# Optimization experiments

Measured on AMD Instinct MI355X. Metric: run time of the kernel, lower is better.

The kernel has to match this reference:

```python
import jax, jax.numpy as jnp
import numpy as np

N_NODES = 5000
K_POOL = 30
BN_EPS = 1e-5


def setup_inputs() -> dict:
    key = jax.random.key(0)
    ks = jax.random.split(key, 16)
    B, N, Din, C, H, OUT, E = 32, N_NODES, 16, 64, 128, 2, 80000
    F_tot = Din + 3 * C  # concat of input + 3 conv layers = 208
    return {
        "x": jax.random.normal(ks[0], (B, N, Din), jnp.float32),
        "age": jax.random.uniform(ks[1], (B,), jnp.float32) * 100.0,
        "edge_attr": jax.random.uniform(ks[2], (E,), jnp.float32) + 0.1,
        "W0": jax.random.normal(ks[3], (Din, C), jnp.float32) * 0.1,
        "b0": jnp.zeros((C,), jnp.float32),
        "W1": jax.random.normal(ks[4], (C, C), jnp.float32) * 0.1,
        "b1": jnp.zeros((C,), jnp.float32),
        "W2": jax.random.normal(ks[5], (C, C), jnp.float32) * 0.1,
        "b2": jnp.zeros((C,), jnp.float32),
        "g0": jnp.ones((C,), jnp.float32),
        "be0": jnp.zeros((C,), jnp.float32),
        "g1": jnp.ones((C,), jnp.float32),
        "be1": jnp.zeros((C,), jnp.float32),
        "mW0": jax.random.normal(ks[6], (K_POOL * F_tot + 1, H), jnp.float32) * 0.02,
        "mb0": jnp.zeros((H,), jnp.float32),
        "mW1": jax.random.normal(ks[7], (H, OUT), jnp.float32) * 0.1,
        "mb1": jnp.zeros((OUT,), jnp.float32),
        "edge_row": jax.random.randint(ks[8], (E,), 0, N, jnp.int32),
        "edge_col": jax.random.randint(ks[9], (E,), 0, N, jnp.int32),
    }


def _spmm(xw, rows, cols, nv):
    # xw: (B, N, C); out[b, r] = sum_{edges (r,c)} nv * xw[b, c]
    def one(xb):
        return jax.ops.segment_sum(xb[cols] * nv[:, None], rows, num_segments=N_NODES)
    return jax.vmap(one)(xw)


def reference(x, age, edge_attr, W0, b0, W1, b1, W2, b2, g0, be0, g1, be1,
              mW0, mb0, mW1, mb1, edge_row, edge_col):
    N = N_NODES
    # GCN normalization on A + I (gcn_norm with edge weights, self-loop value 1)
    loop = jnp.arange(N, dtype=edge_row.dtype)
    rows = jnp.concatenate([edge_row, loop])
    cols = jnp.concatenate([edge_col, loop])
    vals = jnp.concatenate([edge_attr, jnp.ones((N,), edge_attr.dtype)])
    deg = jax.ops.segment_sum(vals, rows, num_segments=N)
    dinv = jnp.where(deg > 0, jax.lax.rsqrt(jnp.maximum(deg, 1e-12)), 0.0)
    nv = dinv[rows] * vals * dinv[cols]

    feats = [x]
    h = x
    convs = [(W0, b0), (W1, b1), (W2, b2)]
    bns = [(g0, be0), (g1, be1)]
    for i, (W, b) in enumerate(convs):
        h = _spmm(h @ W, rows, cols, nv) + b  # GCNConv
        if i < len(convs) - 1:
            g, be = bns[i]
            mu = jnp.mean(h, axis=(0, 1))   # BatchNorm1d over flattened (B*N, C)
            var = jnp.var(h, axis=(0, 1))
            h = (h - mu) * jax.lax.rsqrt(var + BN_EPS) * g + be
        h = jax.nn.relu(h)  # dropout p=0.0 -> identity
        feats.append(h)

    z = jnp.concatenate(feats, axis=-1)  # (B, N, 208)
    # global_sort_pool: sort nodes by last feature channel, descending, take top-k
    order = jnp.argsort(-z[:, :, -1], axis=1)[:, :K_POOL]  # (B, k)
    zk = jnp.take_along_axis(z, order[:, :, None], axis=1)  # (B, k, 208)
    flat = zk.reshape(z.shape[0], -1)
    flat = jnp.concatenate([flat, age[:, None]], axis=1)  # append age scalar

    hm = jax.nn.relu(flat @ mW0 + mb0)  # MLP head
    out = hm @ mW1 + mb1
    return jax.nn.log_softmax(out, axis=-1)
```

## Files before the change

kernel.cpp:

```cpp
#include <hip/hip_runtime.h>
#include <math.h>

#define NN    5000
#define NE    80000
#define NB    32
#define DIN   16
#define CH    64
#define KPOOL 30
#define FTOT  208
#define FLATW 6241
#define NH    128
#define NG    8
#define GB    4
#define NPB   16
#define NCHUNK 313
#define NPAD  5008
#define NEPAD (NE + 4 * NN)
#define NSLOT 32



__global__ void k_init(float* deg, int* counts, float* stats, float* hm, int* perm) {
    int i = blockIdx.x * 256 + threadIdx.x;
    if (i < NN) { deg[i] = 1.0f; counts[i] = 0; }
    if (i < 2 * NSLOT * 128) stats[i] = 0.0f;
    if (i < 4096) hm[i] = 0.0f;
    if (i >= NN && i < NPAD) perm[i] = NN;
}

#define NEB 313
__global__ void k_edges(const float* __restrict__ attr, const int* __restrict__ erow,
                        float* deg, int* counts) {
    int e = blockIdx.x * 256 + threadIdx.x;
    if (e < NE) {
        int r = erow[e];
        atomicAdd(&deg[r], attr[e]);
        atomicAdd(&counts[r], 1);
    }
}

__global__ __launch_bounds__(1024) void k_phase1(
        const int* __restrict__ counts, const float* __restrict__ deg,
        int* rowptr, int* cursor, float* dinv, int* perm,
        const float* __restrict__ x, float* __restrict__ xt) {
    __shared__ int wsum[16], woff[16];
    __shared__ int carry_sh;
    __shared__ int hist[256];
    int t = threadIdx.x;
    if (blockIdx.x >= 2) {
        int idx = (blockIdx.x - 2) * 1024 + t;
        if (idx >= NB * NN) return;
        int b = idx / NN, n = idx % NN;
        int g = b >> 2, bi = b & 3;
        const float4* src = (const float4*)(x + (size_t)idx * DIN);
        float4* dst = (float4*)(xt + (((size_t)g * NN + n) * GB + bi) * DIN);
        dst[0] = src[0]; dst[1] = src[1]; dst[2] = src[2]; dst[3] = src[3];
        return;
    }
    if (blockIdx.x == 0) {
        int lane = t & 63, wid = t >> 6;
        if (t == 0) carry_sh = 0;
        __syncthreads();
        for (int base = 0; base < NN; base += 1024) {
            int carry = carry_sh;
            int i = base + t;
            int v = 0;
            if (i < NN) {
                v = (counts[i] + 3) & ~3;
                dinv[i] = 1.0f / sqrtf(deg[i]);
            }
            int s = v;
#pragma unroll
            for (int off = 1; off < 64; off <<= 1) {
                int o = __shfl_up(s, off);
                if (lane >= off) s += o;
            }
            if (lane == 63) wsum[wid] = s;
            __syncthreads();
            if (t < 16) {
                int w = wsum[t];
#pragma unroll
                for (int off = 1; off < 16; off <<= 1) {
                    int o = __shfl_up(w, off);
                    if (t >= off) w += o;
                }
                woff[t] = w;
            }
            __syncthreads();
            int inc = s + (wid > 0 ? woff[wid - 1] : 0) + carry;
            if (i < NN) {
                rowptr[i + 1] = inc;
                cursor[i] = inc - v;
            }
            if (t == 1023) carry_sh = carry + woff[15];
            __syncthreads();
        }
        if (t == 0) rowptr[0] = 0;
    } else {
        if (t < 256) hist[t] = 0;
        __syncthreads();
        for (int i = t; i < NN; i += 1024) {
            int b = 255 - min(((counts[i] + 3) & ~3) >> 2, 255);
            atomicAdd(&hist[b], 1);
        }
        __syncthreads();
        int mycnt = (t < 256) ? hist[t] : 0;
        for (int off = 1; off < 256; off <<= 1) {
            int v = (t < 256 && t >= off) ? hist[t - off] : 0;
            __syncthreads();
            if (t < 256) hist[t] += v;
            __syncthreads();
        }
        if (t < 256) hist[t] -= mycnt;
        __syncthreads();
        for (int i = t; i < NN; i += 1024) {
            int b = 255 - min(((counts[i] + 3) & ~3) >> 2, 255);
            int pos = atomicAdd(&hist[b], 1);
            perm[pos] = i;
        }
    }
}

__global__ __launch_bounds__(1024) void k_build(
        const int* __restrict__ erow, const int* __restrict__ ecol,
        const float* __restrict__ attr, const float* __restrict__ dinv,
        const int* __restrict__ counts, const int* __restrict__ rowptr,
        int* cursor, int* csr_col, float* csr_nv) {
    int t = blockIdx.x * 1024 + threadIdx.x;
    if (t < NE) {
        int r = erow[t], c = ecol[t];
        int pos = atomicAdd(&cursor[r], 1);
        csr_col[pos] = c;
        csr_nv[pos] = dinv[r] * attr[t] * dinv[c];
    } else if (t - NE < NN) {
        int i = t - NE;
        int cnt = counts[i];
        int pcnt = (cnt + 3) & ~3;
        int base = rowptr[i + 1] - pcnt;
        for (int p = base + cnt; p < base + pcnt; ++p) { csr_col[p] = i; csr_nv[p] = 0.0f; }
    }
}

template<int ACT>
__device__ __forceinline__ float4 actv(float4 v, float4 s, float4 t) {
    if (ACT) {
        v.x = fmaxf(fmaf(v.x, s.x, t.x), 0.f);
        v.y = fmaxf(fmaf(v.y, s.y, t.y), 0.f);
        v.z = fmaxf(fmaf(v.z, s.z, t.z), 0.f);
        v.w = fmaxf(fmaf(v.w, s.w, t.w), 0.f);
    }
    return v;
}
__device__ __forceinline__ void fma4(float4& a, float w, float4 v) {
    a.x = fmaf(w, v.x, a.x); a.y = fmaf(w, v.y, a.y);
    a.z = fmaf(w, v.z, a.z); a.w = fmaf(w, v.w, a.w);
}

template<int CIN, int ACT, int STATS, int SCORE>
__global__ __launch_bounds__(256) void k_layer(
        const float* __restrict__ in, const float* __restrict__ bnstats,
        const float* __restrict__ gamma, const float* __restrict__ beta,
        const float* __restrict__ W, const float* __restrict__ bias,
        const int* __restrict__ rowptr, const int* __restrict__ csr_col,
        const float* __restrict__ csr_nv, const float* __restrict__ dinv,
        const int* __restrict__ perm,
        float* __restrict__ out, float* __restrict__ stats,
        float* __restrict__ score) {
    constexpr int ALS = (CIN == 64) ? 68 : 20;
    __shared__ float As[4 * 16 * ALS];
    __shared__ float stl[ACT ? 128 : 4];
    int tid = threadIdx.x;
    int wid = tid >> 6, lane = tid & 63;
    int g = blockIdx.x & 7;
    int nb = (blockIdx.x >> 3) * NPB;
    int base = nb + wid * 4;
    float* Aw = As + wid * 16 * ALS;
    const int4 pid = *(const int4*)(perm + base);

    if (ACT) {
        if (tid < 64) {
            float su = 0.f, qu = 0.f;
#pragma unroll
            for (int s = 0; s < NSLOT; ++s) {
                su += bnstats[s * 128 + tid];
                qu += bnstats[s * 128 + 64 + tid];
            }
            const float inv = 1.0f / (float)(NB * NN);
            float mu = su * inv;
            float var = qu * inv - mu * mu;
            float sc = gamma[tid] / sqrtf(var + 1e-5f);
            stl[tid] = sc;
            stl[64 + tid] = fmaf(-mu, sc, beta[tid]);
        }
        __syncthreads();
    }

    if (CIN == 64) {
        const float4* __restrict__ in4 = (const float4*)in + (size_t)g * NN * 64;
        int c4 = lane & 15, bi = lane >> 4;
        float4 sv = {1.f,1.f,1.f,1.f}, tv = {0.f,0.f,0.f,0.f};
        if (ACT) { sv = ((const float4*)stl)[c4]; tv = ((const float4*)(stl + 64))[c4]; }
#pragma unroll
        for (int pr = 0; pr < 2; ++pr) {
            int id0 = (pr == 0) ? pid.x : pid.z;
            int id1 = (pr == 0) ? pid.y : pid.w;
            bool vn0 = id0 < NN, vn1 = id1 < NN;
            int rc0 = vn0 ? id0 : 0, rc1 = vn1 ? id1 : 0;
            float dd0 = dinv[rc0]; dd0 *= dd0;
            float dd1 = dinv[rc1]; dd1 *= dd1;
            float4 a0 = {0.f,0.f,0.f,0.f}, a1 = {0.f,0.f,0.f,0.f};
            {
                float4 v0 = actv<ACT>(in4[(size_t)rc0 * 64 + lane], sv, tv);
                float4 v1 = actv<ACT>(in4[(size_t)rc1 * 64 + lane], sv, tv);
                if (vn0) { a0.x = dd0 * v0.x; a0.y = dd0 * v0.y; a0.z = dd0 * v0.z; a0.w = dd0 * v0.w; }
                if (vn1) { a1.x = dd1 * v1.x; a1.y = dd1 * v1.y; a1.z = dd1 * v1.z; a1.w = dd1 * v1.w; }
            }
            int p0a = rowptr[rc0], na = vn0 ? (rowptr[rc0 + 1] - p0a) >> 2 : 0;
            int p0b = rowptr[rc1], nbv = vn1 ? (rowptr[rc1 + 1] - p0b) >> 2 : 0;
            int mx = max(na, nbv);
            for (int bb = 0; bb < mx; ++bb) {
                int ea = min(p0a + 4 * bb, NEPAD - 4);
                int eb = min(p0b + 4 * bb, NEPAD - 4);
                bool va = bb < na, vb = bb < nbv;
                int4   ca = *(const int4*)(csr_col + ea);
                float4 wa = *(const float4*)(csr_nv + ea);
                int4   cb = *(const int4*)(csr_col + eb);
                float4 wb = *(const float4*)(csr_nv + eb);
                if (!va) { wa.x = 0.f; wa.y = 0.f; wa.z = 0.f; wa.w = 0.f;
                           ca.x = 0; ca.y = 0; ca.z = 0; ca.w = 0; }
                if (!vb) { wb.x = 0.f; wb.y = 0.f; wb.z = 0.f; wb.w = 0.f;
                           cb.x = 0; cb.y = 0; cb.z = 0; cb.w = 0; }
                float4 u0 = in4[(size_t)ca.x * 64 + lane];
                float4 u1 = in4[(size_t)ca.y * 64 + lane];
                float4 u2 = in4[(size_t)ca.z * 64 + lane];
                float4 u3 = in4[(size_t)ca.w * 64 + lane];
                float4 t0 = in4[(size_t)cb.x * 64 + lane];
                float4 t1 = in4[(size_t)cb.y * 64 + lane];
                float4 t2 = in4[(size_t)cb.z * 64 + lane];
                float4 t3 = in4[(size_t)cb.w * 64 + lane];
                fma4(a0, wa.x, actv<ACT>(u0, sv, tv));
                fma4(a0, wa.y, actv<ACT>(u1, sv, tv));
                fma4(a0, wa.z, actv<ACT>(u2, sv, tv));
                fma4(a0, wa.w, actv<ACT>(u3, sv, tv));
                fma4(a1, wb.x, actv<ACT>(t0, sv, tv));
                fma4(a1, wb.y, actv<ACT>(t1, sv, tv));
                fma4(a1, wb.z, actv<ACT>(t2, sv, tv));
                fma4(a1, wb.w, actv<ACT>(t3, sv, tv));
            }
            *(float4*)(Aw + ((pr * 2 + 0) * 4 + bi) * ALS + c4 * 4) = a0;
            *(float4*)(Aw + ((pr * 2 + 1) * 4 + bi) * ALS + c4 * 4) = a1;
        }
    } else {
        const float* __restrict__ inr = in + (size_t)g * NN * 64;
        int ids[4] = {pid.x, pid.y, pid.z, pid.w};
#pragma unroll
        for (int i = 0; i < 4; ++i) {
            int r = ids[i];
            float a = 0.f;
            if (r < NN) {
                float d = dinv[r];
                a = d * d * inr[(size_t)r * 64 + lane];
                int p0 = rowptr[r], p1 = rowptr[r + 1];
                for (int e = p0; e < p1; e += 4) {
                    int4   cc = *(const int4*)(csr_col + e);
                    float4 ww = *(const float4*)(csr_nv + e);
                    float v0 = inr[(size_t)cc.x * 64 + lane];
                    float v1 = inr[(size_t)cc.y * 64 + lane];
                    float v2 = inr[(size_t)cc.z * 64 + lane];
                    float v3 = inr[(size_t)cc.w * 64 + lane];
                    a = fmaf(ww.x, v0, a);
                    a = fmaf(ww.y, v1, a);
                    a = fmaf(ww.z, v2, a);
                    a = fmaf(ww.w, v3, a);
                }
            }
            Aw[(i * 4 + (lane >> 4)) * ALS + (lane & 15)] = a;
        }
    }

    int colq = lane & 15, rowq = lane >> 4;
    int node = (rowq == 0) ? pid.x : (rowq == 1) ? pid.y : (rowq == 2) ? pid.z : pid.w;

    if (!SCORE) {
        const float4* __restrict__ W4 = (const float4*)W;
        float4 bb = ((const float4*)bias)[colq];
        float4 o[4];
#pragma unroll
        for (int i = 0; i < 4; ++i) o[i] = bb;
#pragma unroll 8
        for (int k = 0; k < CIN; ++k) {
            float4 w4 = W4[k * 16 + colq];
#pragma unroll
            for (int i = 0; i < 4; ++i) {
                float a = Aw[(rowq * 4 + i) * ALS + k];
                fma4(o[i], a, w4);
            }
        }
        if (node < NN) {
            float4* __restrict__ op = (float4*)(out + ((size_t)g * NN + node) * 256);
#pragma unroll
            for (int i = 0; i < 4; ++i) op[i * 16 + colq] = o[i];
        }

        if (STATS) {
            float4 s4 = {0,0,0,0}, q4 = {0,0,0,0};
            if (node < NN) {
#pragma unroll
                for (int i = 0; i < 4; ++i) {
                    s4.x += o[i].x; s4.y += o[i].y; s4.z += o[i].z; s4.w += o[i].w;
                    q4.x = fmaf(o[i].x, o[i].x, q4.x); q4.y = fmaf(o[i].y, o[i].y, q4.y);
                    q4.z = fmaf(o[i].z, o[i].z, q4.z); q4.w = fmaf(o[i].w, o[i].w, q4.w);
                }
            }
            s4.x += __shfl_xor(s4.x, 16); s4.y += __shfl_xor(s4.y, 16);
            s4.z += __shfl_xor(s4.z, 16); s4.w += __shfl_xor(s4.w, 16);
            q4.x += __shfl_xor(q4.x, 16); q4.y += __shfl_xor(q4.y, 16);
            q4.z += __shfl_xor(q4.z, 16); q4.w += __shfl_xor(q4.w, 16);
            s4.x += __shfl_xor(s4.x, 32); s4.y += __shfl_xor(s4.y, 32);
            s4.z += __shfl_xor(s4.z, 32); s4.w += __shfl_xor(s4.w, 32);
            q4.x += __shfl_xor(q4.x, 32); q4.y += __shfl_xor(q4.y, 32);
            q4.w += __shfl_xor(q4.w, 32); q4.z += __shfl_xor(q4.z, 32);
            __syncthreads();
            if (lane < 16) {
                float* S = As + wid * 128;
                *(float4*)(S + lane * 8) = s4;
                *(float4*)(S + lane * 8 + 4) = q4;
            }
            __syncthreads();
            if (tid < 64) {
                int cq = tid >> 2, comp = tid & 3;
                float s = 0.f, q = 0.f;
#pragma unroll
                for (int w = 0; w < 4; ++w) {
                    s += As[w * 128 + cq * 8 + comp];
                    q += As[w * 128 + cq * 8 + 4 + comp];
                }
                float* sl = stats + (blockIdx.x & (NSLOT - 1)) * 128;
                atomicAdd(&sl[tid], s);
                atomicAdd(&sl[64 + tid], q);
            }
        }
    } else {
        if (node < NN) {
            float4* __restrict__ op = (float4*)(out + ((size_t)g * NN + node) * 256);
#pragma unroll
            for (int i = 0; i < 4; ++i)
                op[i * 16 + colq] = *(const float4*)(Aw + (rowq * 4 + i) * ALS + colq * 4);
        }
        if (lane < 16) {
            int q = lane >> 2;
            int nd = (q == 0) ? pid.x : (q == 1) ? pid.y : (q == 2) ? pid.z : pid.w;
            if (nd < NN) {
                float s = bias[63];
                const float* Ar = Aw + lane * ALS;
#pragma unroll 8
                for (int k = 0; k < 64; ++k)
                    s = fmaf(Ar[k], W[k * 64 + 63], s);
                score[((size_t)g * NN + nd) * 4 + (lane & 3)] = fmaxf(s, 0.f);
            }
        }
    }
}

__global__ __launch_bounds__(1024) void k_toppool(const float* __restrict__ sc, int* order,
        const float* __restrict__ stats,
        const float* __restrict__ g0, const float* __restrict__ be0,
        const float* __restrict__ g1, const float* __restrict__ be1,
        float* __restrict__ st) {
    __shared__ unsigned long long wbest[16];
    __shared__ unsigned long long winner;
    int tid = threadIdx.x;
    if (blockIdx.x == NB) {
        if (tid < 128) {
            int c = tid & 63, layer = tid >> 6;
            const float* sb = stats + layer * NSLOT * 128;
            float su = 0.f, qu = 0.f;
#pragma unroll
            for (int s = 0; s < NSLOT; ++s) {
                su += sb[s * 128 + c];
                qu += sb[s * 128 + 64 + c];
            }
            const float inv = 1.0f / (float)(NB * NN);
            float mu = su * inv;
            float var = qu * inv - mu * mu;
            float g = layer ? g1[c] : g0[c];
            float be = layer ? be1[c] : be0[c];
            float scv = g / sqrtf(var + 1e-5f);
            st[layer * 128 + c] = scv;
            st[layer * 128 + 64 + c] = fmaf(-mu, scv, be);
        }
        return;
    }
    int b = blockIdx.x;
    int g = b >> 2, bi = b & 3;
    int lane = tid & 63, wid = tid >> 6;
    unsigned long long key[5];
#pragma unroll
    for (int j = 0; j < 5; ++j) {
        int n = tid + j * 1024;
        unsigned long long k = 0;
        if (n < NN) {
            float v = sc[((size_t)g * NN + n) * GB + bi];
            k = ((unsigned long long)__float_as_uint(v) << 32) | (unsigned int)(NN - n);
        }
        key[j] = k;
    }
    for (int k = 0; k < KPOOL; ++k) {
        unsigned long long best = key[0];
#pragma unroll
        for (int j = 1; j < 5; ++j) best = (key[j] > best) ? key[j] : best;
#pragma unroll
        for (int off = 1; off < 64; off <<= 1) {
            unsigned long long o = __shfl_xor(best, off);
            best = (o > best) ? o : best;
        }
        if (lane == 0) wbest[wid] = best;
        __syncthreads();
        if (tid == 0) {
            unsigned long long w = wbest[0];
#pragma unroll
            for (int i = 1; i < 16; ++i) w = (wbest[i] > w) ? wbest[i] : w;
            winner = w;
            order[b * KPOOL + k] = NN - (int)(w & 0xFFFFFFFFu);
        }
        __syncthreads();
        int n = NN - (int)(winner & 0xFFFFFFFFu);
        if ((n & 1023) == tid) key[n >> 10] = 0;
    }
}

__global__ void k_gather(const float* __restrict__ xt, const float* __restrict__ h1,
                         const float* __restrict__ h2, const float* __restrict__ agg,
                         const float* __restrict__ W2, const float* __restrict__ b2,
                         const float* __restrict__ st, const float* __restrict__ age,
                         const int* __restrict__ order, float* __restrict__ flat) {
    int bk = blockIdx.x;
    int b = bk / KPOOL, k = bk % KPOOL;
    int n = order[bk];
    int g = b >> 2, bi = b & 3;
    size_t node = (size_t)g * NN + n;
    int f = threadIdx.x;
    float val = 0.f;
    if (f < DIN) {
        val = xt[(node * GB + bi) * DIN + f];
    } else if (f < DIN + CH) {
        int c = f - DIN;
        val = fmaxf(fmaf(h1[(node * GB + bi) * CH + c], st[c], st[64 + c]), 0.f);
    } else if (f < DIN + 2 * CH) {
        int c = f - DIN - CH;
        val = fmaxf(fmaf(h2[(node * GB + bi) * CH + c], st[128 + c], st[192 + c]), 0.f);
    } else if (f < FTOT) {
        int c = f - DIN - 2 * CH;
        const float* __restrict__ Ar = agg + (node * GB + bi) * CH;
        float s = b2[c];
#pragma unroll 8
        for (int kk = 0; kk < 64; ++kk)
            s = fmaf(Ar[kk], W2[kk * 64 + c], s);
        val = fmaxf(s, 0.f);
    }
    if (f < FTOT) flat[(size_t)b * FLATW + k * FTOT + f] = val;
    if (bk == 0 && f >= FTOT && f < FTOT + NB)
        flat[(size_t)(f - FTOT) * FLATW + (FLATW - 1)] = age[f - FTOT];
}

__global__ void k_head1(const float* __restrict__ flat, const float* __restrict__ mW0,
                        float* hm) {
    int tid = threadIdx.x;
    int j4 = (tid & 31) * 4;
    int b0 = (tid >> 5) * 4;
    int kbase = blockIdx.x * 64;
    float acc[4][4];
#pragma unroll
    for (int i = 0; i < 4; i++)
#pragma unroll
        for (int jj = 0; jj < 4; jj++) acc[i][jj] = 0.f;
    int kend = FLATW - kbase; if (kend > 64) kend = 64;
    for (int kk = 0; kk < kend; ++kk) {
        int k = kbase + kk;
        float4 w = *(const float4*)(mW0 + (size_t)k * NH + j4);
#pragma unroll
        for (int i = 0; i < 4; i++) {
            float fv = flat[(size_t)(b0 + i) * FLATW + k];
            acc[i][0] = fmaf(fv, w.x, acc[i][0]);
            acc[i][1] = fmaf(fv, w.y, acc[i][1]);
            acc[i][2] = fmaf(fv, w.z, acc[i][2]);
            acc[i][3] = fmaf(fv, w.w, acc[i][3]);
        }
    }
#pragma unroll
    for (int i = 0; i < 4; i++)
#pragma unroll
        for (int jj = 0; jj < 4; jj++)
            atomicAdd(&hm[(size_t)(b0 + i) * NH + j4 + jj], acc[i][jj]);
}

__global__ void k_head2(const float* __restrict__ hm, const float* __restrict__ mb0,
                        const float* __restrict__ mW1, const float* __restrict__ mb1,
                        float* __restrict__ out) {
    __shared__ float part[256];
    __shared__ float vals[64];
    int tid = threadIdx.x;
    int q = tid & 3, o = (tid >> 2) & 1, b = tid >> 3;
    float acc = 0.f;
    for (int j = q * 32; j < q * 32 + 32; ++j) {
        float hv = fmaxf(hm[b * NH + j] + mb0[j], 0.f);
        acc = fmaf(hv, mW1[j * 2 + o], acc);
    }
    part[tid] = acc;
    __syncthreads();
    if (tid < 64) {
        int b2 = tid >> 1, o2 = tid & 1;
        int base = (b2 << 3) + (o2 << 2);
        vals[tid] = part[base] + part[base + 1] + part[base + 2] + part[base + 3] + mb1[o2];
    }
    __syncthreads();
    if (tid < 64) {
        int b2 = tid >> 1;
        float v0 = vals[b2 * 2], v1 = vals[b2 * 2 + 1];
        float m = fmaxf(v0, v1);
        float lse = m + logf(expf(v0 - m) + expf(v1 - m));
        out[tid] = vals[tid] - lse;
    }
}

extern "C" void kernel_launch(void* const* d_in, const int* in_sizes, int n_in,
                              void* d_out, int out_size, void* d_ws, size_t ws_size,
                              hipStream_t stream) {
    const float* x    = (const float*)d_in[0];
    const float* age  = (const float*)d_in[1];
    const float* attr = (const float*)d_in[2];
    const float* W0   = (const float*)d_in[3];
    const float* b0   = (const float*)d_in[4];
    const float* W1   = (const float*)d_in[5];
    const float* b1   = (const float*)d_in[6];
    const float* W2   = (const float*)d_in[7];
    const float* b2   = (const float*)d_in[8];
    const float* g0   = (const float*)d_in[9];
    const float* be0  = (const float*)d_in[10];
    const float* g1   = (const float*)d_in[11];
    const float* be1  = (const float*)d_in[12];
    const float* mW0  = (const float*)d_in[13];
    const float* mb0  = (const float*)d_in[14];
    const float* mW1  = (const float*)d_in[15];
    const float* mb1  = (const float*)d_in[16];
    const int* erow   = (const int*)d_in[17];
    const int* ecol   = (const int*)d_in[18];
    float* out = (float*)d_out;

    float* ws     = (float*)d_ws;
    float* deg    = ws;
    float* dinv   = deg + 5008;
    int*   counts = (int*)(dinv + 5008);
    int*   rowptr = counts + 5008;
    int*   cursor = rowptr + 5008;
    int*   perm   = cursor + 5008;
    int*   csr_col= perm + 5008;
    float* csr_nv = (float*)(csr_col + NEPAD);
    float* stats  = csr_nv + NEPAD;
    float* st     = stats + 2 * NSLOT * 128;
    float* sc     = st + 256;
    int*   order  = (int*)(sc + NB * NN);
    float* flat   = (float*)(order + 960);
    float* hm     = flat + (size_t)NB * FLATW;
    float* xt     = hm + 4096;
    float* h1     = xt + (size_t)NB * NN * DIN;
    float* h2     = h1 + (size_t)NB * NN * CH;
    float* agg    = h2 + (size_t)NB * NN * CH;

    k_init<<<32, 256, 0, stream>>>(deg, counts, stats, hm, perm);
    k_edges<<<NEB, 256, 0, stream>>>(attr, erow, deg, counts);
    k_phase1<<<2 + (NB * NN + 1023) / 1024, 1024, 0, stream>>>(counts, deg, rowptr, cursor, dinv, perm, x, xt);
    k_build<<<(NE + NN + 1023) / 1024, 1024, 0, stream>>>(erow, ecol, attr, dinv, counts, rowptr, cursor, csr_col, csr_nv);

    const int NBLK = NCHUNK * NG;
    k_layer<16, 0, 1, 0><<<NBLK, 256, 0, stream>>>(xt, nullptr, nullptr, nullptr, W0, b0, rowptr, csr_col, csr_nv, dinv, perm, h1, stats, nullptr);
    k_layer<64, 1, 1, 0><<<NBLK, 256, 0, stream>>>(h1, stats, g0, be0, W1, b1, rowptr, csr_col, csr_nv, dinv, perm, h2, stats + NSLOT * 128, nullptr);
    k_layer<64, 1, 0, 1><<<NBLK, 256, 0, stream>>>(h2, stats + NSLOT * 128, g1, be1, W2, b2, rowptr, csr_col, csr_nv, dinv, perm, agg, nullptr, sc);

    k_toppool<<<NB + 1, 1024, 0, stream>>>(sc, order, stats, g0, be0, g1, be1, st);
    k_gather<<<NB * KPOOL, 256, 0, stream>>>(xt, h1, h2, agg, W2, b2, st, age, order, flat);
    k_head1<<<(FLATW + 63) / 64, 256, 0, stream>>>(flat, mW0, hm);
    k_head2<<<1, 256, 0, stream>>>(hm, mb0, mW1, mb1, out);
}
```

Baseline: 348.6 us.

## Compute sort score via projected channel before SpMM, recompute layer-3 only for top-k

The third GCN layer is no longer run in full. The code first projects the normalized layer-2 activations onto the last column of W2, giving one scalar per node, then runs a scalar SpMM over the CSR to get the sort score. The full 64-channel aggregation for layer 3 is recomputed inside the gather kernel, only for the selected top-k nodes. This removes a full 64-channel SpMM pass and the write of the agg tensor. In exchange it adds two light kernels and per-node neighbour aggregation in the gather kernel, and the different summation order may slightly change scores near ties.

```diff
diff --git a/kernel.cpp b/kernel.cpp
--- a/kernel.cpp
+++ b/kernel.cpp
@@ -156,7 +156,7 @@
     a.z = fmaf(w, v.z, a.z); a.w = fmaf(w, v.w, a.w);
 }
 
-template<int CIN, int ACT, int STATS, int SCORE>
+template<int CIN, int ACT, int STATS>
 __global__ __launch_bounds__(256) void k_layer(
         const float* __restrict__ in, const float* __restrict__ bnstats,
         const float* __restrict__ gamma, const float* __restrict__ beta,
@@ -164,8 +164,7 @@
         const int* __restrict__ rowptr, const int* __restrict__ csr_col,
         const float* __restrict__ csr_nv, const float* __restrict__ dinv,
         const int* __restrict__ perm,
-        float* __restrict__ out, float* __restrict__ stats,
-        float* __restrict__ score) {
+        float* __restrict__ out, float* __restrict__ stats) {
     constexpr int ALS = (CIN == 64) ? 68 : 20;
     __shared__ float As[4 * 16 * ALS];
     __shared__ float stl[ACT ? 128 : 4];
@@ -281,84 +280,151 @@
     int colq = lane & 15, rowq = lane >> 4;
     int node = (rowq == 0) ? pid.x : (rowq == 1) ? pid.y : (rowq == 2) ? pid.z : pid.w;
 
-    if (!SCORE) {
-        const float4* __restrict__ W4 = (const float4*)W;
-        float4 bb = ((const float4*)bias)[colq];
-        float4 o[4];
-#pragma unroll
-        for (int i = 0; i < 4; ++i) o[i] = bb;
+    const float4* __restrict__ W4 = (const float4*)W;
+    float4 bb = ((const float4*)bias)[colq];
+    float4 o[4];
+#pragma unroll
+    for (int i = 0; i < 4; ++i) o[i] = bb;
 #pragma unroll 8
-        for (int k = 0; k < CIN; ++k) {
-            float4 w4 = W4[k * 16 + colq];
+    for (int k = 0; k < CIN; ++k) {
+        float4 w4 = W4[k * 16 + colq];
+#pragma unroll
+        for (int i = 0; i < 4; ++i) {
+            float a = Aw[(rowq * 4 + i) * ALS + k];
+            fma4(o[i], a, w4);
+        }
+    }
+    if (node < NN) {
+        float4* __restrict__ op = (float4*)(out + ((size_t)g * NN + node) * 256);
+#pragma unroll
+        for (int i = 0; i < 4; ++i) op[i * 16 + colq] = o[i];
+    }
+
+    if (STATS) {
+        float4 s4 = {0,0,0,0}, q4 = {0,0,0,0};
+        if (node < NN) {
 #pragma unroll
             for (int i = 0; i < 4; ++i) {
-                float a = Aw[(rowq * 4 + i) * ALS + k];
-                fma4(o[i], a, w4);
-            }
-        }
-        if (node < NN) {
-            float4* __restrict__ op = (float4*)(out + ((size_t)g * NN + node) * 256);
-#pragma unroll
-            for (int i = 0; i < 4; ++i) op[i * 16 + colq] = o[i];
-        }
-
-        if (STATS) {
-            float4 s4 = {0,0,0,0}, q4 = {0,0,0,0};
-            if (node < NN) {
-#pragma unroll
-                for (int i = 0; i < 4; ++i) {
-                    s4.x += o[i].x; s4.y += o[i].y; s4.z += o[i].z; s4.w += o[i].w;
-                    q4.x = fmaf(o[i].x, o[i].x, q4.x); q4.y = fmaf(o[i].y, o[i].y, q4.y);
-                    q4.z = fmaf(o[i].z, o[i].z, q4.z); q4.w = fmaf(o[i].w, o[i].w, q4.w);
-                }
-            }
-            s4.x += __shfl_xor(s4.x, 16); s4.y += __shfl_xor(s4.y, 16);
-            s4.z += __shfl_xor(s4.z, 16); s4.w += __shfl_xor(s4.w, 16);
-            q4.x += __shfl_xor(q4.x, 16); q4.y += __shfl_xor(q4.y, 16);
-            q4.z += __shfl_xor(q4.z, 16); q4.w += __shfl_xor(q4.w, 16);
-            s4.x += __shfl_xor(s4.x, 32); s4.y += __shfl_xor(s4.y, 32);
-            s4.z += __shfl_xor(s4.z, 32); s4.w += __shfl_xor(s4.w, 32);
-            q4.x += __shfl_xor(q4.x, 32); q4.y += __shfl_xor(q4.y, 32);
-            q4.w += __shfl_xor(q4.w, 32); q4.z += __shfl_xor(q4.z, 32);
-            __syncthreads();
-            if (lane < 16) {
-                float* S = As + wid * 128;
-                *(float4*)(S + lane * 8) = s4;
-                *(float4*)(S + lane * 8 + 4) = q4;
-            }
-            __syncthreads();
-            if (tid < 64) {
-                int cq = tid >> 2, comp = tid & 3;
-                float s = 0.f, q = 0.f;
-#pragma unroll
-                for (int w = 0; w < 4; ++w) {
-                    s += As[w * 128 + cq * 8 + comp];
-                    q += As[w * 128 + cq * 8 + 4 + comp];
-                }
-                float* sl = stats + (blockIdx.x & (NSLOT - 1)) * 128;
-                atomicAdd(&sl[tid], s);
-                atomicAdd(&sl[64 + tid], q);
-            }
-        }
-    } else {
-        if (node < NN) {
-            float4* __restrict__ op = (float4*)(out + ((size_t)g * NN + node) * 256);
-#pragma unroll
-            for (int i = 0; i < 4; ++i)
-                op[i * 16 + colq] = *(const float4*)(Aw + (rowq * 4 + i) * ALS + colq * 4);
-        }
+                s4.x += o[i].x; s4.y += o[i].y; s4.z += o[i].z; s4.w += o[i].w;
+                q4.x = fmaf(o[i].x, o[i].x, q4.x); q4.y = fmaf(o[i].y, o[i].y, q4.y);
+                q4.z = fmaf(o[i].z, o[i].z, q4.z); q4.w = fmaf(o[i].w, o[i].w, q4.w);
+            }
+        }
+        s4.x += __shfl_xor(s4.x, 16); s4.y += __shfl_xor(s4.y, 16);
+        s4.z += __shfl_xor(s4.z, 16); s4.w += __shfl_xor(s4.w, 16);
+        q4.x += __shfl_xor(q4.x, 16); q4.y += __shfl_xor(q4.y, 16);
+        q4.z += __shfl_xor(q4.z, 16); q4.w += __shfl_xor(q4.w, 16);
+        s4.x += __shfl_xor(s4.x, 32); s4.y += __shfl_xor(s4.y, 32);
+        s4.z += __shfl_xor(s4.z, 32); s4.w += __shfl_xor(s4.w, 32);
+        q4.x += __shfl_xor(q4.x, 32); q4.y += __shfl_xor(q4.y, 32);
+        q4.z += __shfl_xor(q4.z, 32); q4.w += __shfl_xor(q4.w, 32);
+        __syncthreads();
         if (lane < 16) {
-            int q = lane >> 2;
-            int nd = (q == 0) ? pid.x : (q == 1) ? pid.y : (q == 2) ? pid.z : pid.w;
-            if (nd < NN) {
-                float s = bias[63];
-                const float* Ar = Aw + lane * ALS;
-#pragma unroll 8
-                for (int k = 0; k < 64; ++k)
-                    s = fmaf(Ar[k], W[k * 64 + 63], s);
-                score[((size_t)g * NN + nd) * 4 + (lane & 3)] = fmaxf(s, 0.f);
-            }
-        }
+            float* S = As + wid * 128;
+            *(float4*)(S + lane * 8) = s4;
+            *(float4*)(S + lane * 8 + 4) = q4;
+        }
+        __syncthreads();
+        if (tid < 64) {
+            int cq = tid >> 2, comp = tid & 3;
+            float s = 0.f, q = 0.f;
+#pragma unroll
+            for (int w = 0; w < 4; ++w) {
+                s += As[w * 128 + cq * 8 + comp];
+                q += As[w * 128 + cq * 8 + 4 + comp];
+            }
+            float* sl = stats + (blockIdx.x & (NSLOT - 1)) * 128;
+            atomicAdd(&sl[tid], s);
+            atomicAdd(&sl[64 + tid], q);
+        }
+    }
+}
+
+#define ZBLK 2048
+__global__ __launch_bounds__(256) void k_z(
+        const float* __restrict__ h2, const float* __restrict__ bnstats,
+        const float* __restrict__ gamma, const float* __restrict__ beta,
+        const float* __restrict__ W2, float* __restrict__ z) {
+    __shared__ float stl[128];
+    __shared__ float w63[64];
+    int tid = threadIdx.x;
+    if (tid < 64) {
+        float su = 0.f, qu = 0.f;
+#pragma unroll
+        for (int s = 0; s < NSLOT; ++s) {
+            su += bnstats[s * 128 + tid];
+            qu += bnstats[s * 128 + 64 + tid];
+        }
+        const float inv = 1.0f / (float)(NB * NN);
+        float mu = su * inv;
+        float var = qu * inv - mu * mu;
+        float sc = gamma[tid] / sqrtf(var + 1e-5f);
+        stl[tid] = sc;
+        stl[64 + tid] = fmaf(-mu, sc, beta[tid]);
+        w63[tid] = W2[tid * 64 + 63];
+    }
+    __syncthreads();
+    int lane = tid & 63, wid = tid >> 6;
+    int c4 = lane & 15;
+    float4 sv = ((const float4*)stl)[c4];
+    float4 tv = ((const float4*)(stl + 64))[c4];
+    float4 w4 = ((const float4*)w63)[c4];
+    const int total = NB * NN;
+    for (int base = blockIdx.x * 16; base < total; base += ZBLK * 16) {
+        int row = base + wid * 4 + (lane >> 4);
+        float s = 0.f;
+        if (row < total) {
+            float4 v = ((const float4*)h2)[(size_t)row * 16 + c4];
+            v.x = fmaxf(fmaf(v.x, sv.x, tv.x), 0.f);
+            v.y = fmaxf(fmaf(v.y, sv.y, tv.y), 0.f);
+            v.z = fmaxf(fmaf(v.z, sv.z, tv.z), 0.f);
+            v.w = fmaxf(fmaf(v.w, sv.w, tv.w), 0.f);
+            s = v.x * w4.x + v.y * w4.y + v.z * w4.z + v.w * w4.w;
+        }
+        s += __shfl_xor(s, 1);
+        s += __shfl_xor(s, 2);
+        s += __shfl_xor(s, 4);
+        s += __shfl_xor(s, 8);
+        if ((lane & 15) == 0 && row < total) z[row] = s;
+    }
+}
+
+__global__ __launch_bounds__(256) void k_score(
+        const float* __restrict__ z, const float* __restrict__ b2,
+        const int* __restrict__ rowptr, const int* __restrict__ csr_col,
+        const float* __restrict__ csr_nv, const float* __restrict__ dinv,
+        float* __restrict__ sc) {
+    int tid = threadIdx.x;
+    int wid = tid >> 6, lane = tid & 63;
+    int g = blockIdx.x & 7;
+    int nd = (blockIdx.x >> 3) * 4 + wid;
+    if (nd >= NN) return;
+    const float4* __restrict__ z4 = (const float4*)z + (size_t)g * NN;
+    int p0 = rowptr[nd], p1 = rowptr[nd + 1];
+    float4 a = {0.f, 0.f, 0.f, 0.f};
+    for (int e = p0 + lane; e < p1; e += 64) {
+        int col = csr_col[e];
+        float nv = csr_nv[e];
+        float4 zv = z4[col];
+        fma4(a, nv, zv);
+    }
+#pragma unroll
+    for (int off = 1; off < 64; off <<= 1) {
+        a.x += __shfl_xor(a.x, off);
+        a.y += __shfl_xor(a.y, off);
+        a.z += __shfl_xor(a.z, off);
+        a.w += __shfl_xor(a.w, off);
+    }
+    if (lane == 0) {
+        float d = dinv[nd]; d *= d;
+        float4 zs = z4[nd];
+        float bb = b2[63];
+        float4 o;
+        o.x = fmaxf(fmaf(d, zs.x, a.x) + bb, 0.f);
+        o.y = fmaxf(fmaf(d, zs.y, a.y) + bb, 0.f);
+        o.z = fmaxf(fmaf(d, zs.z, a.z) + bb, 0.f);
+        o.w = fmaxf(fmaf(d, zs.w, a.w) + bb, 0.f);
+        ((float4*)sc)[(size_t)g * NN + nd] = o;
     }
 }
 
@@ -430,16 +496,42 @@
 }
 
 __global__ void k_gather(const float* __restrict__ xt, const float* __restrict__ h1,
-                         const float* __restrict__ h2, const float* __restrict__ agg,
+                         const float* __restrict__ h2,
                          const float* __restrict__ W2, const float* __restrict__ b2,
                          const float* __restrict__ st, const float* __restrict__ age,
+                         const int* __restrict__ rowptr, const int* __restrict__ csr_col,
+                         const float* __restrict__ csr_nv, const float* __restrict__ dinv,
                          const int* __restrict__ order, float* __restrict__ flat) {
+    __shared__ float aggP[4][64];
+    __shared__ float aggRow[64];
     int bk = blockIdx.x;
     int b = bk / KPOOL, k = bk % KPOOL;
     int n = order[bk];
     int g = b >> 2, bi = b & 3;
     size_t node = (size_t)g * NN + n;
-    int f = threadIdx.x;
+    int tid = threadIdx.x;
+    {
+        int ep = tid >> 6, c = tid & 63;
+        float sc1 = st[128 + c], sh1 = st[192 + c];
+        float a = 0.f;
+        if (ep == 0) {
+            float d = dinv[n];
+            float v = h2[(node * GB + bi) * CH + c];
+            a = d * d * fmaxf(fmaf(v, sc1, sh1), 0.f);
+        }
+        int p0 = rowptr[n], p1 = rowptr[n + 1];
+        for (int e = p0 + ep; e < p1; e += 4) {
+            int col = csr_col[e];
+            float nv = csr_nv[e];
+            float v = h2[(((size_t)g * NN + col) * GB + bi) * CH + c];
+            a += nv * fmaxf(fmaf(v, sc1, sh1), 0.f);
+        }
+        aggP[ep][c] = a;
+    }
+    __syncthreads();
+    if (tid < 64) aggRow[tid] = aggP[0][tid] + aggP[1][tid] + aggP[2][tid] + aggP[3][tid];
+    __syncthreads();
+    int f = tid;
     float val = 0.f;
     if (f < DIN) {
         val = xt[(node * GB + bi) * DIN + f];
@@ -451,11 +543,10 @@
         val = fmaxf(fmaf(h2[(node * GB + bi) * CH + c], st[128 + c], st[192 + c]), 0.f);
     } else if (f < FTOT) {
         int c = f - DIN - 2 * CH;
-        const float* __restrict__ Ar = agg + (node * GB + bi) * CH;
         float s = b2[c];
 #pragma unroll 8
         for (int kk = 0; kk < 64; ++kk)
-            s = fmaf(Ar[kk], W2[kk * 64 + c], s);
+            s = fmaf(aggRow[kk], W2[kk * 64 + c], s);
         val = fmaxf(s, 0.f);
     }
     if (f < FTOT) flat[(size_t)b * FLATW + k * FTOT + f] = val;
@@ -565,7 +656,7 @@
     float* xt     = hm + 4096;
     float* h1     = xt + (size_t)NB * NN * DIN;
     float* h2     = h1 + (size_t)NB * NN * CH;
-    float* agg    = h2 + (size_t)NB * NN * CH;
+    float* z      = h2 + (size_t)NB * NN * CH;
 
     k_init<<<32, 256, 0, stream>>>(deg, counts, stats, hm, perm);
     k_edges<<<NEB, 256, 0, stream>>>(attr, erow, deg, counts);
@@ -573,12 +664,13 @@
     k_build<<<(NE + NN + 1023) / 1024, 1024, 0, stream>>>(erow, ecol, attr, dinv, counts, rowptr, cursor, csr_col, csr_nv);
 
     const int NBLK = NCHUNK * NG;
-    k_layer<16, 0, 1, 0><<<NBLK, 256, 0, stream>>>(xt, nullptr, nullptr, nullptr, W0, b0, rowptr, csr_col, csr_nv, dinv, perm, h1, stats, nullptr);
-    k_layer<64, 1, 1, 0><<<NBLK, 256, 0, stream>>>(h1, stats, g0, be0, W1, b1, rowptr, csr_col, csr_nv, dinv, perm, h2, stats + NSLOT * 128, nullptr);
-    k_layer<64, 1, 0, 1><<<NBLK, 256, 0, stream>>>(h2, stats + NSLOT * 128, g1, be1, W2, b2, rowptr, csr_col, csr_nv, dinv, perm, agg, nullptr, sc);
+    k_layer<16, 0, 1><<<NBLK, 256, 0, stream>>>(xt, nullptr, nullptr, nullptr, W0, b0, rowptr, csr_col, csr_nv, dinv, perm, h1, stats);
+    k_layer<64, 1, 1><<<NBLK, 256, 0, stream>>>(h1, stats, g0, be0, W1, b1, rowptr, csr_col, csr_nv, dinv, perm, h2, stats + NSLOT * 128);
+    k_z<<<ZBLK, 256, 0, stream>>>(h2, stats + NSLOT * 128, g1, be1, W2, z);
+    k_score<<<(NN / 4) * NG, 256, 0, stream>>>(z, b2, rowptr, csr_col, csr_nv, dinv, sc);
 
     k_toppool<<<NB + 1, 1024, 0, stream>>>(sc, order, stats, g0, be0, g1, be1, st);
-    k_gather<<<NB * KPOOL, 256, 0, stream>>>(xt, h1, h2, agg, W2, b2, st, age, order, flat);
+    k_gather<<<NB * KPOOL, 256, 0, stream>>>(xt, h1, h2, W2, b2, st, age, rowptr, csr_col, csr_nv, dinv, order, flat);
     k_head1<<<(FLATW + 63) / 64, 256, 0, stream>>>(flat, mW0, hm);
     k_head2<<<1, 256, 0, stream>>>(hm, mb0, mW1, mb1, out);
 }
```

Result: faster. 316.5 us (-9.2%).
